# Performance work log

Hardware: AMD Instinct MI355X
Metric: run time of the kernel (lower is better)

Reference implementation:

```python
import jax, jax.numpy as jnp
import numpy as np

FEATURE_IN = 4096
FEATURE_OUT = 4096
R = 16
ALPHA = 32.0


def setup_inputs() -> dict:
    key = jax.random.key(0)
    k_x, k_w, k_b, k_a = jax.random.split(key, 4)
    x = jax.random.normal(k_x, (4, 2048, FEATURE_IN), dtype=jnp.float32)
    # base linear (torch nn.Linear): weight [out, in], bias [out]
    bound = 1.0 / np.sqrt(FEATURE_IN)
    w = jax.random.uniform(k_w, (FEATURE_OUT, FEATURE_IN), dtype=jnp.float32, minval=-bound, maxval=bound)
    b = jax.random.uniform(k_b, (FEATURE_OUT,), dtype=jnp.float32, minval=-bound, maxval=bound)
    # lora_a: kaiming uniform over [feature_in, r]; lora_b: zeros -> use small randn so grads are nontrivial? No: faithful init is zeros, but zeros makes LoRA path trivially zero. Use kaiming for a, small random for b to exercise the math.
    gain = np.sqrt(2.0 / (1.0 + 5.0 ** 2))  # kaiming_uniform default a=sqrt(5)
    bound_a = gain * np.sqrt(3.0 / FEATURE_IN)
    lora_a = jax.random.uniform(k_a, (FEATURE_IN, R), dtype=jnp.float32, minval=-bound_a, maxval=bound_a)
    lora_b = jax.random.normal(jax.random.fold_in(key, 7), (R, FEATURE_OUT), dtype=jnp.float32) * 0.01
    return {"x": x, "w": w, "b": b, "lora_a": lora_a, "lora_b": lora_b}


def reference(x, w, b, lora_a, lora_b):
    # base linear: x @ W^T + b
    output1 = jnp.einsum('bsi,oi->bso', x, w) + b
    # faithful to source: materialize (A @ B) [feature_in, feature_out] first,
    # then x @ (A@B), scaled by alpha/r
    ab = jnp.matmul(lora_a, lora_b)  # [feature_in, feature_out]
    output2 = jnp.matmul(x, ab) * (ALPHA / R)
    return output2 + output1
```

## Files before the change

### kernel.cpp

```cpp
#include <hip/hip_runtime.h>
#include <cstdint>
#include <cstddef>

#define FEATURE_IN 4096
#define FEATURE_OUT 4096
#define RNK 16

typedef __bf16 bf16x8_t __attribute__((ext_vector_type(8)));
typedef __bf16 bf16x4_t __attribute__((ext_vector_type(4)));
typedef float f32x4_t __attribute__((ext_vector_type(4)));

#define FW_KB 128
#define FW_NB 32
#define NFUSE 4096
#define NCVTB 2048
#define CVT_THREADS (NCVTB * 256)
#define CVT_CHUNKS 16

__global__ __launch_bounds__(256) void prep_all(const float* __restrict__ x,
                                                uint16_t* __restrict__ xb,
                                                const float* __restrict__ w,
                                                const float* __restrict__ la,
                                                const float* __restrict__ lb,
                                                uint16_t* __restrict__ wf) {
    __shared__ float las[FW_KB * RNK];
    __shared__ float lbs[RNK * FW_NB];

    const int tid = threadIdx.x;

    if (blockIdx.x >= NFUSE) {
        const int tg = (blockIdx.x - NFUSE) * 256 + tid;
        const f32x4_t* xp = (const f32x4_t*)x;
        bf16x4_t* op = (bf16x4_t*)xb;
#pragma unroll
        for (int i = 0; i < CVT_CHUNKS; ++i) {
            const int idx = i * CVT_THREADS + tg;
            f32x4_t v = xp[idx];
            bf16x4_t o;
            o[0] = (__bf16)v[0]; o[1] = (__bf16)v[1];
            o[2] = (__bf16)v[2]; o[3] = (__bf16)v[3];
            op[idx] = o;
        }
        return;
    }

    const int bid = blockIdx.x;
    const int kb = (bid & 31) * FW_KB;
    const int nb = (bid >> 5) * FW_NB;

    {
        const float4* src = (const float4*)(la + (size_t)kb * RNK);
        float4* dst = (float4*)las;
        dst[tid] = src[tid];
        dst[tid + 256] = src[tid + 256];
    }
#pragma unroll
    for (int f = tid; f < RNK * FW_NB; f += 256) {
        int r = f >> 5;
        int nl = f & 31;
        lbs[r * FW_NB + nl] = lb[(size_t)r * FEATURE_OUT + nb + nl];
    }
    __syncthreads();

    const int nl = tid >> 3;
    const int kq = tid & 7;

    f32x4_t bcol[4];
#pragma unroll
    for (int r4 = 0; r4 < 4; ++r4) {
        f32x4_t v;
#pragma unroll
        for (int j = 0; j < 4; ++j) v[j] = lbs[(r4 * 4 + j) * FW_NB + nl];
        bcol[r4] = v;
    }

    const f32x4_t* las4 = (const f32x4_t*)las;
    const float* wrow = w + (size_t)(nb + nl) * FEATURE_IN + kb + kq * 16;
    uint16_t* wfrow = wf + (size_t)(nb + nl) * FEATURE_IN + kb + kq * 16;

#pragma unroll
    for (int h = 0; h < 2; ++h) {
        float4 wv0 = ((const float4*)wrow)[h * 2 + 0];
        float4 wv1 = ((const float4*)wrow)[h * 2 + 1];
        float wfv[8] = {wv0.x, wv0.y, wv0.z, wv0.w, wv1.x, wv1.y, wv1.z, wv1.w};
        bf16x8_t o;
#pragma unroll
        for (int j = 0; j < 8; ++j) {
            const int k = kq * 16 + h * 8 + j;
            float s = 0.f;
#pragma unroll
            for (int rr = 0; rr < 4; ++rr) {
                const int r4 = (rr + kq) & 3;
                f32x4_t av = las4[k * 4 + r4];
                f32x4_t bv = bcol[r4];
                s += av[0] * bv[0] + av[1] * bv[1] + av[2] * bv[2] + av[3] * bv[3];
            }
            o[j] = (__bf16)(wfv[j] + 2.f * s);
        }
        ((bf16x8_t*)wfrow)[h] = o;
    }
}

#define BM 256
#define BN 256
#define BK 32
#define NT (FEATURE_IN / BK)

#define ABUF(b) ((b) * 32768)
#define BBUF(b) ((b) * 32768 + 16384)

#define MFMA16X(S) do { _Pragma("unroll")                                                \
    for (int _mi = 0; _mi < 4; ++_mi) { _Pragma("unroll")                                \
        for (int _ni = 0; _ni < 4; ++_ni)                                                \
            acc[_mi][_ni] = __builtin_amdgcn_mfma_f32_16x16x32_bf16(                     \
                afx[S][_mi], bqr[S][_ni], acc[_mi][_ni], 0, 0, 0); } } while (0)

#define MFMA16Y(S) do { _Pragma("unroll")                                                \
    for (int _mi = 0; _mi < 4; ++_mi) { _Pragma("unroll")                                \
        for (int _ni = 0; _ni < 4; ++_ni)                                                \
            acc[4 + _mi][_ni] = __builtin_amdgcn_mfma_f32_16x16x32_bf16(                 \
                afy[_mi], bqr[S][_ni], acc[4 + _mi][_ni], 0, 0, 0); } } while (0)

#define READ_AFY(b) do { _Pragma("unroll")                                               \
    for (int _mi = 0; _mi < 4; ++_mi)                                                    \
        afy[_mi] = *(const bf16x8_t*)(lds + ABUF(b) + aoff[4 + _mi]); } while (0)

#define READ_R0(b, SN) do { _Pragma("unroll")                                            \
    for (int _mi = 0; _mi < 4; ++_mi)                                                    \
        afx[SN][_mi] = *(const bf16x8_t*)(lds + ABUF(b) + aoff[_mi]);                    \
    _Pragma("unroll")                                                                    \
    for (int _ni = 0; _ni < 4; ++_ni)                                                    \
        bqr[SN][_ni] = *(const bf16x8_t*)(lds + BBUF(b) + boff[_ni]); } while (0)

#define GLL(SRC, DSTOFF)                                                                 \
    __builtin_amdgcn_global_load_lds(                                                    \
        (const __attribute__((address_space(1))) void*)(SRC),                            \
        (__attribute__((address_space(3))) void*)(lds + (DSTOFF) + wv * 1024), 16, 0, 0)

#define STAGE_A(b) do { GLL(pA0, ABUF(b)); GLL(pA1, ABUF(b) + 8192);                     \
                        pA0 += BK; pA1 += BK; } while (0)
#define STAGE_B(b) do { GLL(pB0, BBUF(b)); GLL(pB1, BBUF(b) + 8192);                     \
                        pB0 += BK; pB1 += BK; } while (0)

#define PBAR() __builtin_amdgcn_s_barrier()
#define PRIO1 __builtin_amdgcn_s_setprio(1)
#define PRIO0 __builtin_amdgcn_s_setprio(0)
#define VMCNT(n) asm volatile("s_waitcnt vmcnt(" #n ")" ::: "memory")
#define SCHEDB() __builtin_amdgcn_sched_barrier(0)

#define TILE_BODY(CUR, NXT, S, SN)                                                       \
    READ_AFY(CUR);                                                                       \
    STAGE_A(NXT);                                                                        \
    SCHEDB();                                                                            \
    PRIO1; MFMA16X(S); PRIO0;                                                            \
    VMCNT(6);                                                                            \
    PBAR();                                                                              \
    READ_R0((CUR + 1) & 3, SN);                                                          \
    STAGE_B(NXT);                                                                        \
    SCHEDB();                                                                            \
    PRIO1; MFMA16Y(S); PRIO0;                                                            \
    PBAR();

#define TAIL_BODY(CUR, S, SN, NWAIT)                                                     \
    READ_AFY(CUR);                                                                       \
    SCHEDB();                                                                            \
    PRIO1; MFMA16X(S); PRIO0;                                                            \
    VMCNT(NWAIT);                                                                        \
    PBAR();                                                                              \
    READ_R0((CUR + 1) & 3, SN);                                                          \
    SCHEDB();                                                                            \
    PRIO1; MFMA16Y(S); PRIO0;                                                            \
    PBAR();

__global__ __launch_bounds__(512, 2) void gemm256(const uint16_t* __restrict__ Au,
                                                  const uint16_t* __restrict__ Bu,
                                                  const float* __restrict__ bias,
                                                  float* __restrict__ C,
                                                  int M, int N, int K, int mOff) {
    __shared__ __align__(16) char lds[131072];

    const __bf16* A = (const __bf16*)Au;
    const __bf16* B = (const __bf16*)Bu;

    const int tid  = threadIdx.x;
    const int wv   = tid >> 6;
    const int lane = tid & 63;
    const int waveM = wv >> 2;
    const int waveN = wv & 3;
    const int l15 = lane & 15;
    const int q   = lane >> 4;

    const int nbx = N / BN;
    const int nwg = nbx * gridDim.y;
    const int bidlin = blockIdx.y * nbx + blockIdx.x;
    const int swz = (bidlin & 7) * (nwg >> 3) + (bidlin >> 3);
    const int by = swz / nbx;
    const int bx = swz - by * nbx;
    const int m0 = mOff + by * BM;
    const int n0 = bx * BN;

    const int srow = tid >> 2;
    const int sq   = ((tid & 3) - (srow >> 1)) & 3;
    const __bf16* pA0 = A + (size_t)(m0 + srow) * K + sq * 8;
    const __bf16* pA1 = pA0 + (size_t)128 * K;
    const __bf16* pB0 = B + (size_t)(n0 + srow) * K + sq * 8;
    const __bf16* pB1 = pB0 + (size_t)128 * K;

    int aoff[8], boff[4];
#pragma unroll
    for (int mi = 0; mi < 8; ++mi) {
        int row = waveM * 128 + mi * 16 + l15;
        aoff[mi] = row * 64 + (((row >> 1) + q) & 3) * 16;
    }
#pragma unroll
    for (int ni = 0; ni < 4; ++ni) {
        int row = waveN * 64 + ni * 16 + l15;
        boff[ni] = row * 64 + (((row >> 1) + q) & 3) * 16;
    }

    f32x4_t acc[8][4];
#pragma unroll
    for (int mi = 0; mi < 8; ++mi)
#pragma unroll
        for (int ni = 0; ni < 4; ++ni)
            acc[mi][ni] = (f32x4_t)0.f;

    bf16x8_t afx[2][4], afy[4], bqr[2][4];

    STAGE_A(0); STAGE_B(0);
    STAGE_A(1); STAGE_B(1);
    STAGE_A(2); STAGE_B(2);
    VMCNT(8);
    PBAR();
    READ_R0(0, 0);

#pragma unroll 1
    for (int i = 0; i < 31; ++i) {
        TILE_BODY(0, 3, 0, 1)
        TILE_BODY(1, 0, 1, 0)
        TILE_BODY(2, 1, 0, 1)
        TILE_BODY(3, 2, 1, 0)
    }
    TILE_BODY(0, 3, 0, 1)

    TAIL_BODY(1, 1, 0, 4)
    TAIL_BODY(2, 0, 1, 0)
    READ_AFY(3);
    SCHEDB();
    PRIO1; MFMA16X(1); PRIO0;
    PRIO1; MFMA16Y(1); PRIO0;

#pragma unroll
    for (int ni = 0; ni < 4; ++ni) {
        const int col = n0 + waveN * 64 + ni * 16 + l15;
        const float bv = bias[col];
#pragma unroll
        for (int mi = 0; mi < 8; ++mi) {
            const int row = m0 + waveM * 128 + mi * 16 + q * 4;
            float* op = C + (size_t)row * N + col;
#pragma unroll
            for (int j = 0; j < 4; ++j)
                op[(size_t)j * N] = acc[mi][ni][j] + bv;
        }
    }
}

extern "C" void kernel_launch(void* const* d_in, const int* in_sizes, int n_in,
                              void* d_out, int out_size, void* d_ws, size_t ws_size,
                              hipStream_t stream) {
    const float* x  = (const float*)d_in[0];
    const float* w  = (const float*)d_in[1];
    const float* b  = (const float*)d_in[2];
    const float* la = (const float*)d_in[3];
    const float* lb = (const float*)d_in[4];
    float* out = (float*)d_out;

    const int M = in_sizes[0] / FEATURE_IN;
    const int K = FEATURE_IN;
    const int N = FEATURE_OUT;

    uint16_t* xb = (uint16_t*)d_ws;
    uint16_t* wf = (uint16_t*)((char*)d_ws + (size_t)M * K * 2);

    prep_all<<<NFUSE + NCVTB, 256, 0, stream>>>(x, xb, w, la, lb, wf);

    {
        dim3 grid(N / BN, (M / BM) / 2);
        gemm256<<<grid, 512, 0, stream>>>(xb, wf, b, out, M, N, K, 0);
        gemm256<<<grid, 512, 0, stream>>>(xb, wf, b, out, M, N, K, M / 2);
    }
}
```

Baseline: 517.4 us.

## Shrink GEMM tile to 256x128 with 4 waves, triple-buffered LDS, single launch

The GEMM tile goes from 256x256 with 8 waves to 256x128 with 4 waves. LDS use drops from four 32 KB stages to three 24 KB stages, and the prefetch depth falls from 3 to 2 tiles. The two half-M launches become one launch over the full grid, with the loop rescheduled as 21 iterations of 6 tile bodies plus a tail. The aim is smaller LDS so two blocks fit per CU with higher occupancy, and one less launch. The cost is lower arithmetic intensity per block, more B reloads from global memory, and shallower latency hiding.

```diff
diff --git a/kernel.cpp b/kernel.cpp
--- a/kernel.cpp
+++ b/kernel.cpp
@@ -102,12 +102,12 @@
 }
 
 #define BM 256
-#define BN 256
+#define BN 128
 #define BK 32
 #define NT (FEATURE_IN / BK)
 
-#define ABUF(b) ((b) * 32768)
-#define BBUF(b) ((b) * 32768 + 16384)
+#define ABUF(b) ((b) * 24576)
+#define BBUF(b) ((b) * 24576 + 16384)
 
 #define MFMA16X(S) do { _Pragma("unroll")                                                \
     for (int _mi = 0; _mi < 4; ++_mi) { _Pragma("unroll")                                \
@@ -137,10 +137,13 @@
         (const __attribute__((address_space(1))) void*)(SRC),                            \
         (__attribute__((address_space(3))) void*)(lds + (DSTOFF) + wv * 1024), 16, 0, 0)
 
-#define STAGE_A(b) do { GLL(pA0, ABUF(b)); GLL(pA1, ABUF(b) + 8192);                     \
-                        pA0 += BK; pA1 += BK; } while (0)
-#define STAGE_B(b) do { GLL(pB0, BBUF(b)); GLL(pB1, BBUF(b) + 8192);                     \
-                        pB0 += BK; pB1 += BK; } while (0)
+#define STAGE_A(b) do {                                                                  \
+    GLL(pA0, ABUF(b));         GLL(pA1, ABUF(b) + 4096);                                 \
+    GLL(pA2, ABUF(b) + 8192);  GLL(pA3, ABUF(b) + 12288);                                \
+    pA0 += BK; pA1 += BK; pA2 += BK; pA3 += BK; } while (0)
+#define STAGE_B(b) do {                                                                  \
+    GLL(pB0, BBUF(b));         GLL(pB1, BBUF(b) + 4096);                                 \
+    pB0 += BK; pB1 += BK; } while (0)
 
 #define PBAR() __builtin_amdgcn_s_barrier()
 #define PRIO1 __builtin_amdgcn_s_setprio(1)
@@ -148,36 +151,25 @@
 #define VMCNT(n) asm volatile("s_waitcnt vmcnt(" #n ")" ::: "memory")
 #define SCHEDB() __builtin_amdgcn_sched_barrier(0)
 
-#define TILE_BODY(CUR, NXT, S, SN)                                                       \
-    READ_AFY(CUR);                                                                       \
-    STAGE_A(NXT);                                                                        \
+#define TILE_BODY(B, SB, S)                                                              \
+    READ_AFY(B);                                                                         \
+    STAGE_A(SB);                                                                         \
     SCHEDB();                                                                            \
     PRIO1; MFMA16X(S); PRIO0;                                                            \
-    VMCNT(6);                                                                            \
+    VMCNT(4);                                                                            \
     PBAR();                                                                              \
-    READ_R0((CUR + 1) & 3, SN);                                                          \
-    STAGE_B(NXT);                                                                        \
+    READ_R0((B + 1) % 3, (S) ^ 1);                                                       \
+    STAGE_B(SB);                                                                         \
     SCHEDB();                                                                            \
     PRIO1; MFMA16Y(S); PRIO0;                                                            \
     PBAR();
 
-#define TAIL_BODY(CUR, S, SN, NWAIT)                                                     \
-    READ_AFY(CUR);                                                                       \
-    SCHEDB();                                                                            \
-    PRIO1; MFMA16X(S); PRIO0;                                                            \
-    VMCNT(NWAIT);                                                                        \
-    PBAR();                                                                              \
-    READ_R0((CUR + 1) & 3, SN);                                                          \
-    SCHEDB();                                                                            \
-    PRIO1; MFMA16Y(S); PRIO0;                                                            \
-    PBAR();
-
-__global__ __launch_bounds__(512, 2) void gemm256(const uint16_t* __restrict__ Au,
+__global__ __launch_bounds__(256, 2) void gemm256(const uint16_t* __restrict__ Au,
                                                   const uint16_t* __restrict__ Bu,
                                                   const float* __restrict__ bias,
                                                   float* __restrict__ C,
-                                                  int M, int N, int K, int mOff) {
-    __shared__ __align__(16) char lds[131072];
+                                                  int M, int N, int K) {
+    __shared__ __align__(16) char lds[73728];
 
     const __bf16* A = (const __bf16*)Au;
     const __bf16* B = (const __bf16*)Bu;
@@ -185,26 +177,28 @@
     const int tid  = threadIdx.x;
     const int wv   = tid >> 6;
     const int lane = tid & 63;
-    const int waveM = wv >> 2;
-    const int waveN = wv & 3;
+    const int waveM = wv >> 1;
+    const int waveN = wv & 1;
     const int l15 = lane & 15;
     const int q   = lane >> 4;
 
     const int nbx = N / BN;
-    const int nwg = nbx * gridDim.y;
+    const int nwg = nbx * (M / BM);
     const int bidlin = blockIdx.y * nbx + blockIdx.x;
     const int swz = (bidlin & 7) * (nwg >> 3) + (bidlin >> 3);
     const int by = swz / nbx;
     const int bx = swz - by * nbx;
-    const int m0 = mOff + by * BM;
+    const int m0 = by * BM;
     const int n0 = bx * BN;
 
     const int srow = tid >> 2;
     const int sq   = ((tid & 3) - (srow >> 1)) & 3;
     const __bf16* pA0 = A + (size_t)(m0 + srow) * K + sq * 8;
-    const __bf16* pA1 = pA0 + (size_t)128 * K;
+    const __bf16* pA1 = pA0 + (size_t)64 * K;
+    const __bf16* pA2 = pA0 + (size_t)128 * K;
+    const __bf16* pA3 = pA0 + (size_t)192 * K;
     const __bf16* pB0 = B + (size_t)(n0 + srow) * K + sq * 8;
-    const __bf16* pB1 = pB0 + (size_t)128 * K;
+    const __bf16* pB1 = pB0 + (size_t)64 * K;
 
     int aoff[8], boff[4];
 #pragma unroll
@@ -229,23 +223,30 @@
 
     STAGE_A(0); STAGE_B(0);
     STAGE_A(1); STAGE_B(1);
-    STAGE_A(2); STAGE_B(2);
-    VMCNT(8);
+    VMCNT(6);
     PBAR();
     READ_R0(0, 0);
 
 #pragma unroll 1
-    for (int i = 0; i < 31; ++i) {
-        TILE_BODY(0, 3, 0, 1)
-        TILE_BODY(1, 0, 1, 0)
-        TILE_BODY(2, 1, 0, 1)
-        TILE_BODY(3, 2, 1, 0)
-    }
-    TILE_BODY(0, 3, 0, 1)
-
-    TAIL_BODY(1, 1, 0, 4)
-    TAIL_BODY(2, 0, 1, 0)
-    READ_AFY(3);
+    for (int i = 0; i < 21; ++i) {
+        TILE_BODY(0, 2, 0)
+        TILE_BODY(1, 0, 1)
+        TILE_BODY(2, 1, 0)
+        TILE_BODY(0, 2, 1)
+        TILE_BODY(1, 0, 0)
+        TILE_BODY(2, 1, 1)
+    }
+
+    READ_AFY(0);
+    SCHEDB();
+    PRIO1; MFMA16X(0); PRIO0;
+    VMCNT(0);
+    PBAR();
+    READ_R0(1, 1);
+    SCHEDB();
+    PRIO1; MFMA16Y(0); PRIO0;
+    PBAR();
+    READ_AFY(1);
     SCHEDB();
     PRIO1; MFMA16X(1); PRIO0;
     PRIO1; MFMA16Y(1); PRIO0;
@@ -285,8 +286,7 @@
     prep_all<<<NFUSE + NCVTB, 256, 0, stream>>>(x, xb, w, la, lb, wf);
 
     {
-        dim3 grid(N / BN, (M / BM) / 2);
-        gemm256<<<grid, 512, 0, stream>>>(xb, wf, b, out, M, N, K, 0);
-        gemm256<<<grid, 512, 0, stream>>>(xb, wf, b, out, M, N, K, M / 2);
+        dim3 grid(N / BN, M / BM);
+        gemm256<<<grid, 256, 0, stream>>>(xb, wf, b, out, M, N, K);
     }
 }
```

Result: slower. 545.5 us (+5.4%).
